# Kernel optimization log

Hardware: AMD Instinct MI355X
Metric: run time of the kernel (lower is better)

## Reference

```python
import jax, jax.numpy as jnp
import numpy as np

PS = 8          # patch_size
NF = 16         # n_feats
B, H, W = 4, 256, 256
C = NF * PS * PS          # channel_num = 1024
INNER = 3 * C             # heads * channel_num (no head split in source)
SCALE = C ** -0.5         # heads_feats = channel_num
EPS = 1e-5


def _patch(x, shift):
    # reflect-pad then non-overlapping unfold (kernel=PS, stride=PS)
    s = PS // 4
    p = shift * s
    x = jnp.pad(x, ((0, 0), (0, 0), (p, PS - p), (p, PS - p)), mode='reflect')
    b, c, hp, wp = x.shape
    x = x.reshape(b, c, hp // PS, PS, wp // PS, PS)
    # F.unfold ordering: (c, kh, kw) flattened per patch, patches row-major
    x = x.transpose(0, 2, 4, 1, 3, 5).reshape(b, (hp // PS) * (wp // PS), c * PS * PS)
    return x  # [B, N, C*PS*PS]


def _unpatch(x, h, w):
    # inverse of non-overlapping unfold, then crop right/bottom by PS
    b, n, d = x.shape
    c = d // (PS * PS)
    nh, nw = (h + PS) // PS, (w + PS) // PS
    x = x.reshape(b, nh, nw, c, PS, PS).transpose(0, 3, 1, 4, 2, 5)
    x = x.reshape(b, c, nh * PS, nw * PS)
    return x[:, :, :h, :w]


def _ln(x, g, b):
    m = x.mean(-1, keepdims=True)
    v = ((x - m) ** 2).mean(-1, keepdims=True)
    return (x - m) / jnp.sqrt(v + EPS) * g + b


def setup_inputs():
    key = jax.random.key(0)
    ks = jax.random.split(key, 16)
    w = lambda k, shp: jax.random.normal(k, shp, jnp.float32) * 0.02
    return {
        'dr_img': jax.random.normal(ks[0], (B, NF, H, W), jnp.float32),
        'dr_ref': jax.random.normal(ks[1], (B, NF, H, W), jnp.float32),
        'cl_ref': jax.random.normal(ks[2], (B, NF, H, W), jnp.float32),
        'ln_g': jnp.ones((C,), jnp.float32), 'ln_b': jnp.zeros((C,), jnp.float32),
        'Wq': w(ks[3], (C, INNER)), 'bq': jnp.zeros((INNER,), jnp.float32),
        'Wk': w(ks[4], (C, INNER)), 'bk': jnp.zeros((INNER,), jnp.float32),
        'Wv': w(ks[5], (C, INNER)), 'bv': jnp.zeros((INNER,), jnp.float32),
        'Wo': w(ks[6], (INNER, C)), 'bo': jnp.zeros((C,), jnp.float32),
        'ff_ln_g': jnp.ones((C,), jnp.float32), 'ff_ln_b': jnp.zeros((C,), jnp.float32),
        'W1': w(ks[7], (C, C)), 'b1': jnp.zeros((C,), jnp.float32),
        'W2': w(ks[8], (C, C)), 'b2': jnp.zeros((C,), jnp.float32),
    }


def reference(dr_img, dr_ref, cl_ref, ln_g, ln_b, Wq, bq, Wk, bk, Wv, bv,
              Wo, bo, ff_ln_g, ff_ln_b, W1, b1, W2, b2):
    def attn(q, k, v):
        qp = _ln(q, ln_g, ln_b) @ Wq + bq          # [B,N,3C]
        kp = _ln(k, ln_g, ln_b) @ Wk + bk
        vp = _ln(v, ln_g, ln_b) @ Wv + bv
        a = jax.nn.softmax(jnp.einsum('bnd,bmd->bnm', qp, kp) * SCALE, axis=-1)
        return jnp.einsum('bnm,bmd->bnd', a, vp) @ Wo + bo

    def ff(x):
        h = _ln(x, ff_ln_g, ff_ln_b)
        return jax.nn.gelu(h @ W1 + b1, approximate=False) @ W2 + b2

    x = _patch(dr_img, 0)                           # [B,N,C]
    for shift in range(4):
        k = jax.lax.stop_gradient(_patch(dr_ref, shift))
        v = jax.lax.stop_gradient(_patch(cl_ref, shift))
        x = attn(x, k, v) + x
        x = ff(x) + x
    return _unpatch(x, H, W)
```

## Files before the change

kernel.cpp:

```cpp
#include <hip/hip_runtime.h>

typedef unsigned short u16;
typedef float f32x4 __attribute__((ext_vector_type(4)));
typedef __bf16 bf16v8 __attribute__((ext_vector_type(8)));
typedef u16 u16x4 __attribute__((ext_vector_type(4)));

#define WAITV(n) asm volatile("s_waitcnt vmcnt(" #n ")" ::: "memory")
#define TOPBAR() asm volatile("s_barrier" ::: "memory")
#define ENDBAR() asm volatile("s_waitcnt lgkmcnt(0)\n\ts_barrier" ::: "memory")

__device__ __forceinline__ u16 f2bf(float f) {
  union { float f; unsigned int u; } v; v.f = f;
  unsigned int x = v.u;
  x += 0x7fffu + ((x >> 16) & 1u);
  return (u16)(x >> 16);
}

__device__ __forceinline__ int refl(int i, int n) {
  i = (i < 0) ? -i : i;
  return (i >= n) ? (2 * n - 2 - i) : i;
}

__device__ __forceinline__ void gload_lds16(const void* g, void* l) {
  __builtin_amdgcn_global_load_lds(
      (const __attribute__((address_space(1))) void*)g,
      (__attribute__((address_space(3))) void*)l, 16, 0, 0);
}

enum { EPI_BF16_BIAS = 0, EPI_F32 = 1, EPI_BF16 = 2, EPI_F32_RES = 3, EPI_GELU = 4 };

__device__ __forceinline__ void xcd_remap(int& bx, int& by, int& bz) {
  const int gx = gridDim.x, gy = gridDim.y;
  const int nwg = gx * gy * (int)gridDim.z;
  const int orig = ((int)blockIdx.z * gy + (int)blockIdx.y) * gx + (int)blockIdx.x;
  const int q = nwg >> 3, r = nwg & 7;
  const int xcd = orig & 7, loc = orig >> 3;
  const int swz = (xcd < r ? xcd * (q + 1) : r * (q + 1) + (xcd - r) * q) + loc;
  const int gxy = gx * gy;
  bz = swz / gxy;
  const int rem = swz - bz * gxy;
  by = rem / gx; bx = rem - by * gx;
}

template <int EPI>
__global__ __launch_bounds__(512, 2) void gemm256(
    const u16* __restrict__ A, const u16* __restrict__ Bt, void* __restrict__ Cp,
    const float* __restrict__ bias, int K, int Nld, long sA, long sB, long sC, long sBias)
{
  extern __shared__ __align__(16) u16 smem[];
  u16* As = smem;
  u16* Bs = smem + 32768;

  const int t = threadIdx.x;
  int bx, by, bz; xcd_remap(bx, by, bz);
  const int m0 = by * 256, n0 = bx * 256;

  const long Kb = (long)K * 2;
  const int sc = ((t & 7) * 16) ^ (((t >> 3) & 7) << 4);
  const char* Ag = (const char*)(A + (long)bz * sA + (long)m0 * K) + (long)(t >> 3) * Kb + sc;
  const char* Bg = (const char*)(Bt + (long)bz * sB + (long)n0 * K) + (long)(t >> 3) * Kb + sc;

  auto STAGE = [&](int d, int kt) {
    const long ko = (long)kt * 128;
#pragma unroll
    for (int i = 0; i < 4; i++)
      gload_lds16(Ag + (long)i * 64 * Kb + ko, &As[d * 16384 + i * 4096 + t * 8]);
#pragma unroll
    for (int i = 0; i < 4; i++)
      gload_lds16(Bg + (long)i * 64 * Kb + ko, &Bs[d * 16384 + i * 4096 + t * 8]);
  };

  const int w = t >> 6, lane = t & 63;
  const int wm = (w >> 2) * 128, wn = (w & 3) * 64;
  const int lr = lane & 15, hi = lane >> 4;
  const int cx = (lr & 7) << 4;

  f32x4 acc[8][4];
  const f32x4 vzero = {0.f, 0.f, 0.f, 0.f};
#pragma unroll
  for (int i = 0; i < 8; i++)
#pragma unroll
    for (int j = 0; j < 4; j++) acc[i][j] = vzero;

  const int NT = K >> 6;
  STAGE(0, 0);
  STAGE(1, 1);

  for (int kt = 0; kt < NT; kt++) {
    const int d = kt & 1;
    if (kt + 1 < NT) { WAITV(8); } else { WAITV(0); }
    TOPBAR();

    const u16* Ad = &As[d * 16384];
    const u16* Bd = &Bs[d * 16384];
#pragma unroll
    for (int ks = 0; ks < 2; ks++) {
      bf16v8 a8[8], b8[4];
      const int cb = ks * 64;
#pragma unroll
      for (int mi = 0; mi < 8; mi++)
        a8[mi] = *(const bf16v8*)&Ad[(wm + mi * 16 + lr) * 64 + (((cb + hi * 16) ^ cx) >> 1)];
#pragma unroll
      for (int ni = 0; ni < 4; ni++)
        b8[ni] = *(const bf16v8*)&Bd[(wn + ni * 16 + lr) * 64 + (((cb + hi * 16) ^ cx) >> 1)];
      __builtin_amdgcn_s_setprio(1);
#pragma unroll
      for (int mi = 0; mi < 8; mi++)
#pragma unroll
        for (int ni = 0; ni < 4; ni++)
          acc[mi][ni] = __builtin_amdgcn_mfma_f32_16x16x32_bf16(a8[mi], b8[ni], acc[mi][ni], 0, 0, 0);
      __builtin_amdgcn_s_setprio(0);
    }
    ENDBAR();
    if (kt + 2 < NT) STAGE(d, kt + 2);
  }

#pragma unroll
  for (int mi = 0; mi < 8; mi++) {
    const int r0 = m0 + wm + mi * 16 + hi * 4;
#pragma unroll
    for (int ni = 0; ni < 4; ni++) {
      const int col = n0 + wn + ni * 16 + lr;
      float bvv = 0.f;
      if constexpr (EPI == EPI_BF16_BIAS) bvv = bias[bz * sBias + col];
#pragma unroll
      for (int j = 0; j < 4; j++) {
        const long idx = (long)(r0 + j) * Nld + col;
        const float val = acc[mi][ni][j] + bvv;
        if constexpr (EPI == EPI_BF16_BIAS || EPI == EPI_BF16) {
          ((u16*)Cp + (long)bz * sC)[idx] = f2bf(val);
        } else {
          ((float*)Cp + (long)bz * sC)[idx] = val;
        }
      }
    }
  }
}

template <int EPI>
__global__ __launch_bounds__(256, 2) void gemm128(
    const u16* __restrict__ A, const u16* __restrict__ Bt, void* __restrict__ Cp,
    const float* __restrict__ bias, int K, int Nld, long sA, long sB, long sC)
{
  extern __shared__ __align__(16) u16 smem[];
  u16* As = smem;
  u16* Bs = smem + 16384;

  const int t = threadIdx.x;
  int bx, by, bz; xcd_remap(bx, by, bz);
  const int m0 = by * 128, n0 = bx * 128;

  const long Kb = (long)K * 2;
  const int sc = ((t & 7) * 16) ^ (((t >> 3) & 7) << 4);
  const char* Ag = (const char*)(A + (long)bz * sA + (long)m0 * K) + (long)(t >> 3) * Kb + sc;
  const char* Bg = (const char*)(Bt + (long)bz * sB + (long)n0 * K) + (long)(t >> 3) * Kb + sc;

  auto STAGE = [&](int d, int kt) {
    const long ko = (long)kt * 128;
#pragma unroll
    for (int i = 0; i < 4; i++)
      gload_lds16(Ag + (long)i * 32 * Kb + ko, &As[d * 8192 + i * 2048 + t * 8]);
#pragma unroll
    for (int i = 0; i < 4; i++)
      gload_lds16(Bg + (long)i * 32 * Kb + ko, &Bs[d * 8192 + i * 2048 + t * 8]);
  };

  const int w = t >> 6, lane = t & 63;
  const int wm = (w >> 1) * 64, wn = (w & 1) * 64;
  const int lr = lane & 15, hi = lane >> 4;
  const int cx = (lr & 7) << 4;

  f32x4 acc[4][4];
  const f32x4 vzero = {0.f, 0.f, 0.f, 0.f};
#pragma unroll
  for (int i = 0; i < 4; i++)
#pragma unroll
    for (int j = 0; j < 4; j++) acc[i][j] = vzero;

  const int NT = K >> 6;
  STAGE(0, 0);
  STAGE(1, 1);

  for (int kt = 0; kt < NT; kt++) {
    const int d = kt & 1;
    if (kt + 1 < NT) { WAITV(8); } else { WAITV(0); }
    TOPBAR();

    const u16* Ad = &As[d * 8192];
    const u16* Bd = &Bs[d * 8192];
#pragma unroll
    for (int ks = 0; ks < 2; ks++) {
      bf16v8 a8[4], b8[4];
      const int cb = ks * 64;
#pragma unroll
      for (int mi = 0; mi < 4; mi++)
        a8[mi] = *(const bf16v8*)&Ad[(wm + mi * 16 + lr) * 64 + (((cb + hi * 16) ^ cx) >> 1)];
#pragma unroll
      for (int ni = 0; ni < 4; ni++)
        b8[ni] = *(const bf16v8*)&Bd[(wn + ni * 16 + lr) * 64 + (((cb + hi * 16) ^ cx) >> 1)];
      __builtin_amdgcn_s_setprio(1);
#pragma unroll
      for (int mi = 0; mi < 4; mi++)
#pragma unroll
        for (int ni = 0; ni < 4; ni++)
          acc[mi][ni] = __builtin_amdgcn_mfma_f32_16x16x32_bf16(a8[mi], b8[ni], acc[mi][ni], 0, 0, 0);
      __builtin_amdgcn_s_setprio(0);
    }
    ENDBAR();
    if (kt + 2 < NT) STAGE(d, kt + 2);
  }

#pragma unroll
  for (int mi = 0; mi < 4; mi++) {
    const int r0 = m0 + wm + mi * 16 + hi * 4;
#pragma unroll
    for (int ni = 0; ni < 4; ni++) {
      const int col = n0 + wn + ni * 16 + lr;
      float bvv = 0.f;
      if constexpr (EPI == EPI_F32_RES || EPI == EPI_GELU) bvv = bias[col];
#pragma unroll
      for (int j = 0; j < 4; j++) {
        const long idx = (long)(r0 + j) * Nld + col;
        const float val = acc[mi][ni][j] + bvv;
        if constexpr (EPI == EPI_F32) {
          ((float*)Cp + (long)bz * sC)[idx] = val;
        } else if constexpr (EPI == EPI_F32_RES) {
          ((float*)Cp)[idx] += val;
        } else if constexpr (EPI == EPI_GELU) {
          const float gv = 0.5f * val * (1.f + erff(val * 0.70710678118654752440f));
          ((u16*)Cp)[idx] = f2bf(gv);
        } else {
          ((u16*)Cp)[idx] = f2bf(val);
        }
      }
    }
  }
}

__global__ __launch_bounds__(256) void ln_kernel(const float* __restrict__ X,
    const float* __restrict__ g, const float* __restrict__ be, u16* __restrict__ Y)
{
  const long row = blockIdx.x;
  const int t = threadIdx.x;
  const float* xr = X + row * 1024;
  f32x4 v = *(const f32x4*)&xr[t * 4];
  float s = v[0] + v[1] + v[2] + v[3];
  float q = v[0]*v[0] + v[1]*v[1] + v[2]*v[2] + v[3]*v[3];
#pragma unroll
  for (int off = 32; off; off >>= 1) { s += __shfl_xor(s, off); q += __shfl_xor(q, off); }
  __shared__ float red[8];
  if ((t & 63) == 0) { red[t >> 6] = s; red[4 + (t >> 6)] = q; }
  __syncthreads();
  s = red[0] + red[1] + red[2] + red[3];
  q = red[4] + red[5] + red[6] + red[7];
  const float mean = s * (1.f / 1024.f);
  const float rstd = rsqrtf(q * (1.f / 1024.f) - mean * mean + 1e-5f);
  f32x4 gv = *(const f32x4*)&g[t * 4];
  f32x4 bv = *(const f32x4*)&be[t * 4];
  u16x4 o;
#pragma unroll
  for (int i = 0; i < 4; i++) o[i] = f2bf((v[i] - mean) * rstd * gv[i] + bv[i]);
  *(u16x4*)&Y[row * 1024 + t * 4] = o;
}

__global__ __launch_bounds__(256) void patch_kernel(const float* __restrict__ img,
    float* __restrict__ X, int shift)
{
  const int n = blockIdx.x, b = blockIdx.y, t = threadIdx.x;
  float* xr = X + ((long)b * 1280 + n) * 1024;
  if (n >= 1089) {
    const f32x4 z = {0.f, 0.f, 0.f, 0.f};
    *(f32x4*)&xr[t * 4] = z;
    return;
  }
  const int p = shift * 2;
  const int ph = n / 33, pw = n - ph * 33;
  const int d0 = t * 4;
  const int c = d0 >> 6, kh = (d0 >> 3) & 7, kw0 = d0 & 7;
  const int hh = refl(ph * 8 + kh - p, 256);
  const float* src = img + ((long)(b * 16 + c) * 256 + hh) * 256;
  f32x4 v;
#pragma unroll
  for (int i = 0; i < 4; i++) v[i] = src[refl(pw * 8 + kw0 + i - p, 256)];
  *(f32x4*)&xr[d0] = v;
}

__global__ __launch_bounds__(256) void patch_ln_kernel(const float* __restrict__ img,
    const float* __restrict__ g, const float* __restrict__ be, u16* __restrict__ Y, int shift)
{
  const int n = blockIdx.x, b = blockIdx.y, t = threadIdx.x;
  u16* yr = Y + ((long)b * 1280 + n) * 1024;
  if (n >= 1089) {
    const u16x4 z = {0, 0, 0, 0};
    *(u16x4*)&yr[t * 4] = z;
    return;
  }
  const int p = shift * 2;
  const int ph = n / 33, pw = n - ph * 33;
  const int d0 = t * 4;
  const int c = d0 >> 6, kh = (d0 >> 3) & 7, kw0 = d0 & 7;
  const int hh = refl(ph * 8 + kh - p, 256);
  const float* src = img + ((long)(b * 16 + c) * 256 + hh) * 256;
  float v[4];
#pragma unroll
  for (int i = 0; i < 4; i++) v[i] = src[refl(pw * 8 + kw0 + i - p, 256)];
  float s = v[0] + v[1] + v[2] + v[3];
  float q = v[0]*v[0] + v[1]*v[1] + v[2]*v[2] + v[3]*v[3];
#pragma unroll
  for (int off = 32; off; off >>= 1) { s += __shfl_xor(s, off); q += __shfl_xor(q, off); }
  __shared__ float red[8];
  if ((t & 63) == 0) { red[t >> 6] = s; red[4 + (t >> 6)] = q; }
  __syncthreads();
  s = red[0] + red[1] + red[2] + red[3];
  q = red[4] + red[5] + red[6] + red[7];
  const float mean = s * (1.f / 1024.f);
  const float rstd = rsqrtf(q * (1.f / 1024.f) - mean * mean + 1e-5f);
  u16x4 o;
#pragma unroll
  for (int i = 0; i < 4; i++) o[i] = f2bf((v[i] - mean) * rstd * g[d0 + i] + be[d0 + i]);
  *(u16x4*)&yr[d0] = o;
}

__global__ __launch_bounds__(256) void softmax_kernel(const float* __restrict__ L,
    u16* __restrict__ P)
{
  const int r = blockIdx.x, b = blockIdx.y, t = threadIdx.x;
  const float* Lr = L + ((long)b * 1280 + r) * 1280;
  u16* Pr = P + ((long)b * 1280 + r) * 1280;
  float v[5];
  float mx = -1e30f;
#pragma unroll
  for (int i = 0; i < 5; i++) {
    const int j = t + i * 256;
    v[i] = (j < 1089) ? Lr[j] * 0.03125f : -1e30f;
    mx = fmaxf(mx, v[i]);
  }
#pragma unroll
  for (int off = 32; off; off >>= 1) mx = fmaxf(mx, __shfl_xor(mx, off));
  __shared__ float sm[4];
  if ((t & 63) == 0) sm[t >> 6] = mx;
  __syncthreads();
  mx = fmaxf(fmaxf(sm[0], sm[1]), fmaxf(sm[2], sm[3]));
  float p[5];
  float s = 0.f;
#pragma unroll
  for (int i = 0; i < 5; i++) {
    const int j = t + i * 256;
    p[i] = (j < 1089) ? __expf(v[i] - mx) : 0.f;
    s += p[i];
  }
#pragma unroll
  for (int off = 32; off; off >>= 1) s += __shfl_xor(s, off);
  __shared__ float ss[4];
  if ((t & 63) == 0) ss[t >> 6] = s;
  __syncthreads();
  const float inv = 1.f / (ss[0] + ss[1] + ss[2] + ss[3]);
#pragma unroll
  for (int i = 0; i < 5; i++) Pr[t + i * 256] = f2bf(p[i] * inv);
}

__global__ __launch_bounds__(256) void vtrans_kernel(const u16* __restrict__ V,
    u16* __restrict__ Vt)
{
  __shared__ u16 tile[32][33];
  const int b = blockIdx.z;
  const int d0 = blockIdx.x * 32, m0 = blockIdx.y * 32;
  const int tx = threadIdx.x & 31, ty = threadIdx.x >> 5;
  const u16* Vb = V + (long)b * 1280 * 3072;
  u16* Vtb = Vt + (long)b * 3072 * 1280;
#pragma unroll
  for (int i = 0; i < 4; i++)
    tile[ty + 8 * i][tx] = Vb[(long)(m0 + ty + 8 * i) * 3072 + d0 + tx];
  __syncthreads();
#pragma unroll
  for (int i = 0; i < 4; i++)
    Vtb[(long)(d0 + ty + 8 * i) * 1280 + m0 + tx] = tile[tx][ty + 8 * i];
}

__global__ __launch_bounds__(256) void wtrans_kernel(const float* __restrict__ W,
    u16* __restrict__ Wt, int K, int N)
{
  __shared__ float tile[32][33];
  const int n0 = blockIdx.x * 32, k0 = blockIdx.y * 32;
  const int tx = threadIdx.x & 31, ty = threadIdx.x >> 5;
#pragma unroll
  for (int i = 0; i < 4; i++)
    tile[ty + 8 * i][tx] = W[(long)(k0 + ty + 8 * i) * N + n0 + tx];
  __syncthreads();
#pragma unroll
  for (int i = 0; i < 4; i++)
    Wt[(long)(n0 + ty + 8 * i) * K + k0 + tx] = f2bf(tile[tx][ty + 8 * i]);
}

__global__ __launch_bounds__(256) void catbias_kernel(const float* __restrict__ a,
    const float* __restrict__ b, const float* __restrict__ c, float* __restrict__ o)
{
  const int i = blockIdx.x * 256 + threadIdx.x;
  o[i] = a[i]; o[3072 + i] = b[i]; o[6144 + i] = c[i];
}

__global__ __launch_bounds__(256) void unpatch_kernel(const float* __restrict__ X,
    float* __restrict__ out)
{
  const int idx = blockIdx.x * 256 + threadIdx.x;
  const int w = (idx & 63) * 4;
  const int h = (idx >> 6) & 255;
  const int c = (idx >> 14) & 15;
  const int b = idx >> 18;
  const int ph = h >> 3, kh = h & 7, pw = w >> 3, kw = w & 7;
  const long row = (long)b * 1280 + ph * 33 + pw;
  const int d = c * 64 + kh * 8 + kw;
  const f32x4 v = *(const f32x4*)&X[row * 1024 + d];
  *(f32x4*)&out[((long)(b * 16 + c) * 256 + h) * 256 + w] = v;
}

extern "C" void kernel_launch(void* const* d_in, const int* in_sizes, int n_in,
                              void* d_out, int out_size, void* d_ws, size_t ws_size,
                              hipStream_t stream)
{
  (void)in_sizes; (void)n_in; (void)out_size; (void)ws_size;
  const float* dr_img = (const float*)d_in[0];
  const float* dr_ref = (const float*)d_in[1];
  const float* cl_ref = (const float*)d_in[2];
  const float* ln_g = (const float*)d_in[3];
  const float* ln_be = (const float*)d_in[4];
  const float* Wq = (const float*)d_in[5];
  const float* bq = (const float*)d_in[6];
  const float* Wk = (const float*)d_in[7];
  const float* bk = (const float*)d_in[8];
  const float* Wv = (const float*)d_in[9];
  const float* bv = (const float*)d_in[10];
  const float* Wo = (const float*)d_in[11];
  const float* bo = (const float*)d_in[12];
  const float* ffg = (const float*)d_in[13];
  const float* ffb = (const float*)d_in[14];
  const float* W1 = (const float*)d_in[15];
  const float* b1 = (const float*)d_in[16];
  const float* W2 = (const float*)d_in[17];
  const float* b2 = (const float*)d_in[18];

  const long R = 1280;
  const long MR = 4 * R;

  char* ws = (char*)d_ws;
  size_t off = 0;
  auto alloc = [&](size_t bytes) -> void* {
    void* pp = ws + off;
    off += (bytes + 255) & ~(size_t)255;
    return pp;
  };
  float* x    = (float*)alloc((size_t)MR * 1024 * 4);
  u16* xkv_ln = (u16*)alloc((size_t)3 * MR * 1024 * 2);
  u16* qkv    = (u16*)alloc((size_t)3 * MR * 3072 * 2);
  float* lgt  = (float*)alloc((size_t)4 * R * R * 4);
  u16* P      = (u16*)alloc((size_t)4 * R * R * 2);
  u16* Wqkv_t = (u16*)alloc((size_t)3 * 3072 * 1024 * 2);
  u16* Wo_t   = (u16*)alloc((size_t)1024 * 3072 * 2);
  u16* W1_t   = (u16*)alloc((size_t)1024 * 1024 * 2);
  u16* W2_t   = (u16*)alloc((size_t)1024 * 1024 * 2);
  float* bcat = (float*)alloc((size_t)3 * 3072 * 4);

  u16* x_ln = xkv_ln;
  u16* h    = xkv_ln + (size_t)MR * 1024;
  u16* qp   = qkv;
  u16* kp   = qkv + (size_t)MR * 3072;
  u16* vp   = qkv + (size_t)2 * MR * 3072;

  wtrans_kernel<<<dim3(96, 32), 256, 0, stream>>>(Wq, Wqkv_t, 1024, 3072);
  wtrans_kernel<<<dim3(96, 32), 256, 0, stream>>>(Wk, Wqkv_t + (size_t)3072 * 1024, 1024, 3072);
  wtrans_kernel<<<dim3(96, 32), 256, 0, stream>>>(Wv, Wqkv_t + (size_t)2 * 3072 * 1024, 1024, 3072);
  wtrans_kernel<<<dim3(32, 96), 256, 0, stream>>>(Wo, Wo_t, 3072, 1024);
  wtrans_kernel<<<dim3(32, 32), 256, 0, stream>>>(W1, W1_t, 1024, 1024);
  wtrans_kernel<<<dim3(32, 32), 256, 0, stream>>>(W2, W2_t, 1024, 1024);
  catbias_kernel<<<12, 256, 0, stream>>>(bq, bk, bv, bcat);

  patch_kernel<<<dim3(1280, 4), 256, 0, stream>>>(dr_img, x, 0);

  const long sAp = (long)MR * 1024;
  const long sBp = (long)3072 * 1024;
  const long sCp = (long)MR * 3072;
  const long sQb = R * 3072;
  const long sLb = R * R;

  for (int shift = 0; shift < 4; shift++) {
    ln_kernel<<<(int)MR, 256, 0, stream>>>(x, ln_g, ln_be, x_ln);
    patch_ln_kernel<<<dim3(1280, 4), 256, 0, stream>>>(dr_ref, ln_g, ln_be, xkv_ln + sAp, shift);
    patch_ln_kernel<<<dim3(1280, 4), 256, 0, stream>>>(cl_ref, ln_g, ln_be, xkv_ln + 2 * sAp, shift);

    gemm256<EPI_BF16_BIAS><<<dim3(12, 20, 3), 512, 131072, stream>>>(
        xkv_ln, Wqkv_t, qkv, bcat, 1024, 3072, sAp, sBp, sCp, 3072);

    gemm128<EPI_F32><<<dim3(10, 10, 4), 256, 65536, stream>>>(
        qp, kp, lgt, nullptr, 3072, 1280, sQb, sQb, sLb);

    softmax_kernel<<<dim3(1280, 4), 256, 0, stream>>>(lgt, P);
    vtrans_kernel<<<dim3(96, 40, 4), 256, 0, stream>>>(vp, kp);

    gemm256<EPI_BF16><<<dim3(12, 5, 4), 512, 131072, stream>>>(
        P, kp, qp, nullptr, 1280, 3072, sLb, (long)3072 * R, sQb, 0);

    gemm128<EPI_F32_RES><<<dim3(8, 40, 1), 256, 65536, stream>>>(
        qp, Wo_t, x, bo, 3072, 1024, 0, 0, 0);

    ln_kernel<<<(int)MR, 256, 0, stream>>>(x, ffg, ffb, x_ln);
    gemm128<EPI_GELU><<<dim3(8, 40, 1), 256, 65536, stream>>>(
        x_ln, W1_t, h, b1, 1024, 1024, 0, 0, 0);
    gemm128<EPI_F32_RES><<<dim3(8, 40, 1), 256, 65536, stream>>>(
        h, W2_t, x, b2, 1024, 1024, 0, 0, 0);
  }

  unpatch_kernel<<<4096, 256, 0, stream>>>(x, (float*)d_out);
}
```

Baseline: 1.533 ms.

## Switch GEMMs to 3-stage LDS ring with K=32 tiles and split A/B staging

Both GEMM kernels move from a double-buffered K=64 tile to a triple-buffered ring of K=32 tiles, with a new 4-chunk XOR swizzle. The next-next stage is issued at the start of each iteration rather than after the compute. gemm256 additionally splits each iteration into two half-M compute phases, interleaving A and B prefetches and LDS fragment loads with barriers. The aim is better overlap of global-to-LDS loads with MFMA work and lower LDS use per block (96KB/48KB). The cost is more barriers per unit of work and shorter MFMA bursts between syncs.

```diff
diff --git a/kernel.cpp b/kernel.cpp
--- a/kernel.cpp
+++ b/kernel.cpp
@@ -6,8 +6,9 @@
 typedef u16 u16x4 __attribute__((ext_vector_type(4)));
 
 #define WAITV(n) asm volatile("s_waitcnt vmcnt(" #n ")" ::: "memory")
-#define TOPBAR() asm volatile("s_barrier" ::: "memory")
-#define ENDBAR() asm volatile("s_waitcnt lgkmcnt(0)\n\ts_barrier" ::: "memory")
+#define BAR() asm volatile("s_barrier" ::: "memory")
+#define LGKM0() do { asm volatile("s_waitcnt lgkmcnt(0)" ::: "memory"); \
+                     __builtin_amdgcn_sched_barrier(0); } while (0)
 
 __device__ __forceinline__ u16 f2bf(float f) {
   union { float f; unsigned int u; } v; v.f = f;
@@ -48,32 +49,32 @@
     const float* __restrict__ bias, int K, int Nld, long sA, long sB, long sC, long sBias)
 {
   extern __shared__ __align__(16) u16 smem[];
-  u16* As = smem;
-  u16* Bs = smem + 32768;
 
   const int t = threadIdx.x;
   int bx, by, bz; xcd_remap(bx, by, bz);
   const int m0 = by * 256, n0 = bx * 256;
 
   const long Kb = (long)K * 2;
-  const int sc = ((t & 7) * 16) ^ (((t >> 3) & 7) << 4);
-  const char* Ag = (const char*)(A + (long)bz * sA + (long)m0 * K) + (long)(t >> 3) * Kb + sc;
-  const char* Bg = (const char*)(Bt + (long)bz * sB + (long)n0 * K) + (long)(t >> 3) * Kb + sc;
-
-  auto STAGE = [&](int d, int kt) {
-    const long ko = (long)kt * 128;
-#pragma unroll
-    for (int i = 0; i < 4; i++)
-      gload_lds16(Ag + (long)i * 64 * Kb + ko, &As[d * 16384 + i * 4096 + t * 8]);
-#pragma unroll
-    for (int i = 0; i < 4; i++)
-      gload_lds16(Bg + (long)i * 64 * Kb + ko, &Bs[d * 16384 + i * 4096 + t * 8]);
+  const int srow = t >> 2;
+  const int schunk = ((t & 3) ^ (srow & 3)) * 16;
+  const char* Ag = (const char*)(A + (long)bz * sA + (long)m0 * K) + (long)srow * Kb + schunk;
+  const char* Bg = (const char*)(Bt + (long)bz * sB + (long)n0 * K) + (long)srow * Kb + schunk;
+
+  auto STAGE_A = [&](int s, int kt) {
+    const long ko = (long)kt * 64;
+    gload_lds16(Ag + ko, &smem[s * 16384 + t * 8]);
+    gload_lds16(Ag + 128 * Kb + ko, &smem[s * 16384 + 4096 + t * 8]);
+  };
+  auto STAGE_B = [&](int s, int kt) {
+    const long ko = (long)kt * 64;
+    gload_lds16(Bg + ko, &smem[s * 16384 + 8192 + t * 8]);
+    gload_lds16(Bg + 128 * Kb + ko, &smem[s * 16384 + 12288 + t * 8]);
   };
 
   const int w = t >> 6, lane = t & 63;
   const int wm = (w >> 2) * 128, wn = (w & 3) * 64;
   const int lr = lane & 15, hi = lane >> 4;
-  const int cx = (lr & 7) << 4;
+  const int rchunk = ((hi ^ (lr & 3)) * 16) >> 1;
 
   f32x4 acc[8][4];
   const f32x4 vzero = {0.f, 0.f, 0.f, 0.f};
@@ -82,37 +83,48 @@
 #pragma unroll
     for (int j = 0; j < 4; j++) acc[i][j] = vzero;
 
-  const int NT = K >> 6;
-  STAGE(0, 0);
-  STAGE(1, 1);
+  const int NT = K >> 5;
+  STAGE_A(0, 0); STAGE_B(0, 0);
+  STAGE_A(1, 1); STAGE_B(1, 1);
+  int c = 0;
 
   for (int kt = 0; kt < NT; kt++) {
-    const int d = kt & 1;
-    if (kt + 1 < NT) { WAITV(8); } else { WAITV(0); }
-    TOPBAR();
-
-    const u16* Ad = &As[d * 16384];
-    const u16* Bd = &Bs[d * 16384];
-#pragma unroll
-    for (int ks = 0; ks < 2; ks++) {
-      bf16v8 a8[8], b8[4];
-      const int cb = ks * 64;
-#pragma unroll
-      for (int mi = 0; mi < 8; mi++)
-        a8[mi] = *(const bf16v8*)&Ad[(wm + mi * 16 + lr) * 64 + (((cb + hi * 16) ^ cx) >> 1)];
+    if (kt + 1 < NT) { WAITV(4); } else { WAITV(0); }
+    BAR();
+    const int s = (c == 0) ? 2 : c - 1;
+    const u16* Ad = &smem[c * 16384];
+    const u16* Bd = &smem[c * 16384 + 8192];
+    bf16v8 a8[4], b8[4];
+
+    if (kt + 2 < NT) STAGE_A(s, kt + 2);
+#pragma unroll
+    for (int i = 0; i < 4; i++) a8[i] = *(const bf16v8*)&Ad[(wm + i * 16 + lr) * 32 + rchunk];
+#pragma unroll
+    for (int i = 0; i < 4; i++) b8[i] = *(const bf16v8*)&Bd[(wn + i * 16 + lr) * 32 + rchunk];
+    BAR();
+    LGKM0();
+    __builtin_amdgcn_s_setprio(1);
+#pragma unroll
+    for (int mi = 0; mi < 4; mi++)
 #pragma unroll
       for (int ni = 0; ni < 4; ni++)
-        b8[ni] = *(const bf16v8*)&Bd[(wn + ni * 16 + lr) * 64 + (((cb + hi * 16) ^ cx) >> 1)];
-      __builtin_amdgcn_s_setprio(1);
-#pragma unroll
-      for (int mi = 0; mi < 8; mi++)
-#pragma unroll
-        for (int ni = 0; ni < 4; ni++)
-          acc[mi][ni] = __builtin_amdgcn_mfma_f32_16x16x32_bf16(a8[mi], b8[ni], acc[mi][ni], 0, 0, 0);
-      __builtin_amdgcn_s_setprio(0);
-    }
-    ENDBAR();
-    if (kt + 2 < NT) STAGE(d, kt + 2);
+        acc[mi][ni] = __builtin_amdgcn_mfma_f32_16x16x32_bf16(a8[mi], b8[ni], acc[mi][ni], 0, 0, 0);
+    __builtin_amdgcn_s_setprio(0);
+    BAR();
+
+    if (kt + 2 < NT) STAGE_B(s, kt + 2);
+#pragma unroll
+    for (int i = 0; i < 4; i++) a8[i] = *(const bf16v8*)&Ad[(wm + 64 + i * 16 + lr) * 32 + rchunk];
+    BAR();
+    LGKM0();
+    __builtin_amdgcn_s_setprio(1);
+#pragma unroll
+    for (int mi = 0; mi < 4; mi++)
+#pragma unroll
+      for (int ni = 0; ni < 4; ni++)
+        acc[4 + mi][ni] = __builtin_amdgcn_mfma_f32_16x16x32_bf16(a8[mi], b8[ni], acc[4 + mi][ni], 0, 0, 0);
+    __builtin_amdgcn_s_setprio(0);
+    c = (c == 2) ? 0 : c + 1;
   }
 
 #pragma unroll
@@ -143,32 +155,29 @@
     const float* __restrict__ bias, int K, int Nld, long sA, long sB, long sC)
 {
   extern __shared__ __align__(16) u16 smem[];
-  u16* As = smem;
-  u16* Bs = smem + 16384;
 
   const int t = threadIdx.x;
   int bx, by, bz; xcd_remap(bx, by, bz);
   const int m0 = by * 128, n0 = bx * 128;
 
   const long Kb = (long)K * 2;
-  const int sc = ((t & 7) * 16) ^ (((t >> 3) & 7) << 4);
-  const char* Ag = (const char*)(A + (long)bz * sA + (long)m0 * K) + (long)(t >> 3) * Kb + sc;
-  const char* Bg = (const char*)(Bt + (long)bz * sB + (long)n0 * K) + (long)(t >> 3) * Kb + sc;
-
-  auto STAGE = [&](int d, int kt) {
-    const long ko = (long)kt * 128;
-#pragma unroll
-    for (int i = 0; i < 4; i++)
-      gload_lds16(Ag + (long)i * 32 * Kb + ko, &As[d * 8192 + i * 2048 + t * 8]);
-#pragma unroll
-    for (int i = 0; i < 4; i++)
-      gload_lds16(Bg + (long)i * 32 * Kb + ko, &Bs[d * 8192 + i * 2048 + t * 8]);
+  const int srow = t >> 2;
+  const int schunk = ((t & 3) ^ (srow & 3)) * 16;
+  const char* Ag = (const char*)(A + (long)bz * sA + (long)m0 * K) + (long)srow * Kb + schunk;
+  const char* Bg = (const char*)(Bt + (long)bz * sB + (long)n0 * K) + (long)srow * Kb + schunk;
+
+  auto STAGE = [&](int s, int kt) {
+    const long ko = (long)kt * 64;
+    gload_lds16(Ag + ko, &smem[s * 8192 + t * 8]);
+    gload_lds16(Ag + 64 * Kb + ko, &smem[s * 8192 + 2048 + t * 8]);
+    gload_lds16(Bg + ko, &smem[s * 8192 + 4096 + t * 8]);
+    gload_lds16(Bg + 64 * Kb + ko, &smem[s * 8192 + 6144 + t * 8]);
   };
 
   const int w = t >> 6, lane = t & 63;
   const int wm = (w >> 1) * 64, wn = (w & 1) * 64;
   const int lr = lane & 15, hi = lane >> 4;
-  const int cx = (lr & 7) << 4;
+  const int rchunk = ((hi ^ (lr & 3)) * 16) >> 1;
 
   f32x4 acc[4][4];
   const f32x4 vzero = {0.f, 0.f, 0.f, 0.f};
@@ -177,37 +186,32 @@
 #pragma unroll
     for (int j = 0; j < 4; j++) acc[i][j] = vzero;
 
-  const int NT = K >> 6;
-  STAGE(0, 0);
-  STAGE(1, 1);
+  const int NT = K >> 5;
+  STAGE(0, 0); STAGE(1, 1);
+  int c = 0;
 
   for (int kt = 0; kt < NT; kt++) {
-    const int d = kt & 1;
-    if (kt + 1 < NT) { WAITV(8); } else { WAITV(0); }
-    TOPBAR();
-
-    const u16* Ad = &As[d * 8192];
-    const u16* Bd = &Bs[d * 8192];
-#pragma unroll
-    for (int ks = 0; ks < 2; ks++) {
-      bf16v8 a8[4], b8[4];
-      const int cb = ks * 64;
-#pragma unroll
-      for (int mi = 0; mi < 4; mi++)
-        a8[mi] = *(const bf16v8*)&Ad[(wm + mi * 16 + lr) * 64 + (((cb + hi * 16) ^ cx) >> 1)];
+    if (kt + 1 < NT) { WAITV(4); } else { WAITV(0); }
+    BAR();
+    const int s = (c == 0) ? 2 : c - 1;
+    const u16* Ad = &smem[c * 8192];
+    const u16* Bd = &smem[c * 8192 + 4096];
+    if (kt + 2 < NT) STAGE(s, kt + 2);
+    bf16v8 a8[4], b8[4];
+#pragma unroll
+    for (int i = 0; i < 4; i++) a8[i] = *(const bf16v8*)&Ad[(wm + i * 16 + lr) * 32 + rchunk];
+#pragma unroll
+    for (int i = 0; i < 4; i++) b8[i] = *(const bf16v8*)&Bd[(wn + i * 16 + lr) * 32 + rchunk];
+    BAR();
+    LGKM0();
+    __builtin_amdgcn_s_setprio(1);
+#pragma unroll
+    for (int mi = 0; mi < 4; mi++)
 #pragma unroll
       for (int ni = 0; ni < 4; ni++)
-        b8[ni] = *(const bf16v8*)&Bd[(wn + ni * 16 + lr) * 64 + (((cb + hi * 16) ^ cx) >> 1)];
-      __builtin_amdgcn_s_setprio(1);
-#pragma unroll
-      for (int mi = 0; mi < 4; mi++)
-#pragma unroll
-        for (int ni = 0; ni < 4; ni++)
-          acc[mi][ni] = __builtin_amdgcn_mfma_f32_16x16x32_bf16(a8[mi], b8[ni], acc[mi][ni], 0, 0, 0);
-      __builtin_amdgcn_s_setprio(0);
-    }
-    ENDBAR();
-    if (kt + 2 < NT) STAGE(d, kt + 2);
+        acc[mi][ni] = __builtin_amdgcn_mfma_f32_16x16x32_bf16(a8[mi], b8[ni], acc[mi][ni], 0, 0, 0);
+    __builtin_amdgcn_s_setprio(0);
+    c = (c == 2) ? 0 : c + 1;
   }
 
 #pragma unroll
@@ -487,25 +491,25 @@
     patch_ln_kernel<<<dim3(1280, 4), 256, 0, stream>>>(dr_ref, ln_g, ln_be, xkv_ln + sAp, shift);
     patch_ln_kernel<<<dim3(1280, 4), 256, 0, stream>>>(cl_ref, ln_g, ln_be, xkv_ln + 2 * sAp, shift);
 
-    gemm256<EPI_BF16_BIAS><<<dim3(12, 20, 3), 512, 131072, stream>>>(
+    gemm256<EPI_BF16_BIAS><<<dim3(12, 20, 3), 512, 98304, stream>>>(
         xkv_ln, Wqkv_t, qkv, bcat, 1024, 3072, sAp, sBp, sCp, 3072);
 
-    gemm128<EPI_F32><<<dim3(10, 10, 4), 256, 65536, stream>>>(
+    gemm128<EPI_F32><<<dim3(10, 10, 4), 256, 49152, stream>>>(
         qp, kp, lgt, nullptr, 3072, 1280, sQb, sQb, sLb);
 
     softmax_kernel<<<dim3(1280, 4), 256, 0, stream>>>(lgt, P);
     vtrans_kernel<<<dim3(96, 40, 4), 256, 0, stream>>>(vp, kp);
 
-    gemm256<EPI_BF16><<<dim3(12, 5, 4), 512, 131072, stream>>>(
+    gemm256<EPI_BF16><<<dim3(12, 5, 4), 512, 98304, stream>>>(
         P, kp, qp, nullptr, 1280, 3072, sLb, (long)3072 * R, sQb, 0);
 
-    gemm128<EPI_F32_RES><<<dim3(8, 40, 1), 256, 65536, stream>>>(
+    gemm128<EPI_F32_RES><<<dim3(8, 40, 1), 256, 49152, stream>>>(
         qp, Wo_t, x, bo, 3072, 1024, 0, 0, 0);
 
     ln_kernel<<<(int)MR, 256, 0, stream>>>(x, ffg, ffb, x_ln);
-    gemm128<EPI_GELU><<<dim3(8, 40, 1), 256, 65536, stream>>>(
+    gemm128<EPI_GELU><<<dim3(8, 40, 1), 256, 49152, stream>>>(
         x_ln, W1_t, h, b1, 1024, 1024, 0, 0, 0);
-    gemm128<EPI_F32_RES><<<dim3(8, 40, 1), 256, 65536, stream>>>(
+    gemm128<EPI_F32_RES><<<dim3(8, 40, 1), 256, 49152, stream>>>(
         h, W2_t, x, b2, 1024, 1024, 0, 0, 0);
   }
 
```

New measurement: 1.614 ms. 1.05x slower.

## Interleave global-to-LDS prefetch into quarter-steps of the 256x256 GEMM main loop

Applied to the files above, without the earlier changes.

Restructures the gemm256 main loop into 8 sub-phases per two k-tiles, each loading a slice of A fragments, issuing part of the next tile's global_load_lds traffic, then doing 16 MFMAs, separated by barriers. The goal is to spread memory issue across the compute so loads overlap MFMA work, instead of issuing a burst of 8 loads after each tile. The swizzle math is rewritten equivalently. It adds many more barriers per iteration and assumes NT is even, which is a correctness risk if K/64 is odd.

```diff
diff --git a/kernel.cpp b/kernel.cpp
--- a/kernel.cpp
+++ b/kernel.cpp
@@ -6,8 +6,9 @@
 typedef u16 u16x4 __attribute__((ext_vector_type(4)));
 
 #define WAITV(n) asm volatile("s_waitcnt vmcnt(" #n ")" ::: "memory")
-#define TOPBAR() asm volatile("s_barrier" ::: "memory")
-#define ENDBAR() asm volatile("s_waitcnt lgkmcnt(0)\n\ts_barrier" ::: "memory")
+#define BAR() asm volatile("s_barrier" ::: "memory")
+#define LGKM0() do { asm volatile("s_waitcnt lgkmcnt(0)" ::: "memory"); \
+                     __builtin_amdgcn_sched_barrier(0); } while (0)
 
 __device__ __forceinline__ u16 f2bf(float f) {
   union { float f; unsigned int u; } v; v.f = f;
@@ -48,32 +49,33 @@
     const float* __restrict__ bias, int K, int Nld, long sA, long sB, long sC, long sBias)
 {
   extern __shared__ __align__(16) u16 smem[];
-  u16* As = smem;
-  u16* Bs = smem + 32768;
 
   const int t = threadIdx.x;
   int bx, by, bz; xcd_remap(bx, by, bz);
   const int m0 = by * 256, n0 = bx * 256;
 
   const long Kb = (long)K * 2;
-  const int sc = ((t & 7) * 16) ^ (((t >> 3) & 7) << 4);
-  const char* Ag = (const char*)(A + (long)bz * sA + (long)m0 * K) + (long)(t >> 3) * Kb + sc;
-  const char* Bg = (const char*)(Bt + (long)bz * sB + (long)n0 * K) + (long)(t >> 3) * Kb + sc;
-
-  auto STAGE = [&](int d, int kt) {
+  const int sr8 = t >> 3;
+  const int schunk = ((t & 7) ^ (sr8 & 7)) * 16;
+  const char* Ag = (const char*)(A + (long)bz * sA + (long)m0 * K) + (long)sr8 * Kb + schunk;
+  const char* Bg = (const char*)(Bt + (long)bz * sB + (long)n0 * K) + (long)sr8 * Kb + schunk;
+
+  auto SA = [&](int d, int kt, int i0, int i1) {
     const long ko = (long)kt * 128;
-#pragma unroll
-    for (int i = 0; i < 4; i++)
-      gload_lds16(Ag + (long)i * 64 * Kb + ko, &As[d * 16384 + i * 4096 + t * 8]);
-#pragma unroll
-    for (int i = 0; i < 4; i++)
-      gload_lds16(Bg + (long)i * 64 * Kb + ko, &Bs[d * 16384 + i * 4096 + t * 8]);
+    gload_lds16(Ag + (long)i0 * 64 * Kb + ko, &smem[d * 32768 + i0 * 4096 + t * 8]);
+    gload_lds16(Ag + (long)i1 * 64 * Kb + ko, &smem[d * 32768 + i1 * 4096 + t * 8]);
+  };
+  auto SB = [&](int d, int kt, int i0, int i1) {
+    const long ko = (long)kt * 128;
+    gload_lds16(Bg + (long)i0 * 64 * Kb + ko, &smem[d * 32768 + 16384 + i0 * 4096 + t * 8]);
+    gload_lds16(Bg + (long)i1 * 64 * Kb + ko, &smem[d * 32768 + 16384 + i1 * 4096 + t * 8]);
   };
 
   const int w = t >> 6, lane = t & 63;
   const int wm = (w >> 2) * 128, wn = (w & 3) * 64;
   const int lr = lane & 15, hi = lane >> 4;
-  const int cx = (lr & 7) << 4;
+  const int rc0 = ((0 * 4 + hi) ^ (lr & 7)) * 8;
+  const int rc1 = ((1 * 4 + hi) ^ (lr & 7)) * 8;
 
   f32x4 acc[8][4];
   const f32x4 vzero = {0.f, 0.f, 0.f, 0.f};
@@ -82,37 +84,67 @@
 #pragma unroll
     for (int j = 0; j < 4; j++) acc[i][j] = vzero;
 
-  const int NT = K >> 6;
-  STAGE(0, 0);
-  STAGE(1, 1);
-
-  for (int kt = 0; kt < NT; kt++) {
-    const int d = kt & 1;
-    if (kt + 1 < NT) { WAITV(8); } else { WAITV(0); }
-    TOPBAR();
-
-    const u16* Ad = &As[d * 16384];
-    const u16* Bd = &Bs[d * 16384];
-#pragma unroll
-    for (int ks = 0; ks < 2; ks++) {
-      bf16v8 a8[8], b8[4];
-      const int cb = ks * 64;
-#pragma unroll
-      for (int mi = 0; mi < 8; mi++)
-        a8[mi] = *(const bf16v8*)&Ad[(wm + mi * 16 + lr) * 64 + (((cb + hi * 16) ^ cx) >> 1)];
-#pragma unroll
-      for (int ni = 0; ni < 4; ni++)
-        b8[ni] = *(const bf16v8*)&Bd[(wn + ni * 16 + lr) * 64 + (((cb + hi * 16) ^ cx) >> 1)];
-      __builtin_amdgcn_s_setprio(1);
-#pragma unroll
-      for (int mi = 0; mi < 8; mi++)
-#pragma unroll
-        for (int ni = 0; ni < 4; ni++)
-          acc[mi][ni] = __builtin_amdgcn_mfma_f32_16x16x32_bf16(a8[mi], b8[ni], acc[mi][ni], 0, 0, 0);
-      __builtin_amdgcn_s_setprio(0);
+  const int NT = K >> 6, NI = NT >> 1;
+
+  SA(0, 0, 0, 1); SA(0, 0, 2, 3); SB(0, 0, 0, 1); SB(0, 0, 2, 3);
+  SB(1, 1, 0, 2); SB(1, 1, 1, 3); SA(1, 1, 0, 2);
+  WAITV(6);
+  BAR();
+
+  for (int i = 0; i < NI; i++) {
+    const int t0 = 2 * i;
+    const bool last = (i == NI - 1);
+#pragma unroll
+    for (int h = 0; h < 2; h++) {
+      const u16* Ad = &smem[h * 32768];
+      const u16* Bd = Ad + 16384;
+      bf16v8 b8[4][2];
+#pragma unroll
+      for (int q = 0; q < 4; q++) {
+        bf16v8 a8[2][2];
+#pragma unroll
+        for (int j = 0; j < 2; j++) {
+          const int rbase = (wm + (2 * q + j) * 16 + lr) * 64;
+          a8[j][0] = *(const bf16v8*)&Ad[rbase + rc0];
+          a8[j][1] = *(const bf16v8*)&Ad[rbase + rc1];
+        }
+        if (q == 0) {
+#pragma unroll
+          for (int ni = 0; ni < 4; ni++) {
+            const int rbase = (wn + ni * 16 + lr) * 64;
+            b8[ni][0] = *(const bf16v8*)&Bd[rbase + rc0];
+            b8[ni][1] = *(const bf16v8*)&Bd[rbase + rc1];
+          }
+        }
+        if (h == 0) {
+          if (q == 0)           SA(1, t0 + 1, 1, 3);
+          else if (!last) {
+            if (q == 1)         SB(0, t0 + 2, 0, 2);
+            else if (q == 2)    SB(0, t0 + 2, 1, 3);
+            else                SA(0, t0 + 2, 0, 2);
+          }
+        } else if (!last) {
+          if (q == 0)           SA(0, t0 + 2, 1, 3);
+          else if (q == 1)      SB(1, t0 + 3, 0, 2);
+          else if (q == 2)      SB(1, t0 + 3, 1, 3);
+          else                  SA(1, t0 + 3, 0, 2);
+        }
+        BAR();
+        LGKM0();
+        __builtin_amdgcn_s_setprio(1);
+#pragma unroll
+        for (int j = 0; j < 2; j++)
+#pragma unroll
+          for (int ni = 0; ni < 4; ni++) {
+            acc[2 * q + j][ni] = __builtin_amdgcn_mfma_f32_16x16x32_bf16(a8[j][0], b8[ni][0], acc[2 * q + j][ni], 0, 0, 0);
+            acc[2 * q + j][ni] = __builtin_amdgcn_mfma_f32_16x16x32_bf16(a8[j][1], b8[ni][1], acc[2 * q + j][ni], 0, 0, 0);
+          }
+        __builtin_amdgcn_s_setprio(0);
+        if (h == 0 && q == 3) { if (last) { WAITV(0); } else { WAITV(6); } }
+        if (h == 1 && q == 3 && !last) { WAITV(6); }
+        BAR();
+      }
     }
-    ENDBAR();
-    if (kt + 2 < NT) STAGE(d, kt + 2);
   }
 
 #pragma unroll
@@ -184,7 +216,7 @@
   for (int kt = 0; kt < NT; kt++) {
     const int d = kt & 1;
     if (kt + 1 < NT) { WAITV(8); } else { WAITV(0); }
-    TOPBAR();
+    BAR();
 
     const u16* Ad = &As[d * 8192];
     const u16* Bd = &Bs[d * 8192];
@@ -206,7 +238,7 @@
           acc[mi][ni] = __builtin_amdgcn_mfma_f32_16x16x32_bf16(a8[mi], b8[ni], acc[mi][ni], 0, 0, 0);
       __builtin_amdgcn_s_setprio(0);
     }
-    ENDBAR();
+    asm volatile("s_waitcnt lgkmcnt(0)\n\ts_barrier" ::: "memory");
     if (kt + 2 < NT) STAGE(d, kt + 2);
   }
 
```

Result: faster. 1.486 ms (-3.1%).
